# Performance work log

Hardware: AMD Instinct MI355X
Metric: run time of the kernel (lower is better)

## Reference

```python
import jax, jax.numpy as jnp
import numpy as np


def setup_inputs() -> dict:
    key = jax.random.key(0)
    ks = jax.random.split(key, 6)
    B, H, T, Dk, Dv = 64, 16, 4, 128, 256
    q = jax.random.normal(ks[0], (B, H, T, Dk), dtype=jnp.float32)
    k = jax.random.normal(ks[1], (B, H, T, Dk), dtype=jnp.float32)
    v = jax.random.normal(ks[2], (B, H, T, Dv), dtype=jnp.float32)
    g = jax.random.uniform(ks[3], (B, H, T), dtype=jnp.float32)
    beta = jax.random.uniform(ks[4], (B, H, T), dtype=jnp.float32)
    last_recurrent_state = jax.random.normal(ks[5], (B, H, Dk, Dv), dtype=jnp.float32)
    return {"q": q, "k": k, "v": v, "g": g, "beta": beta,
            "last_recurrent_state": last_recurrent_state}


def reference(q, k, v, g, beta, last_recurrent_state):
    # q,k: (B,H,T,Dk)  v: (B,H,T,Dv)  g,beta: (B,H,T)  state: (B,H,Dk,Dv)
    def step(state, xs):
        q_t, k_t, v_t, g_t, beta_t = xs  # (B,H,Dk),(B,H,Dk),(B,H,Dv),(B,H),(B,H)
        state = state * jnp.exp(g_t)[..., None, None]           # decay
        kv_mem = jnp.einsum('bhkv,bhk->bhv', state, k_t)         # readout with key
        delta = (v_t - kv_mem) * beta_t[..., None]               # delta-rule correction
        state = state + k_t[..., None] * delta[..., None, :]     # rank-1 update
        out_t = jnp.einsum('bhkv,bhk->bhv', state, q_t)          # query readout
        return state, out_t

    xs = (jnp.moveaxis(q, 2, 0), jnp.moveaxis(k, 2, 0), jnp.moveaxis(v, 2, 0),
          jnp.moveaxis(g, 2, 0), jnp.moveaxis(beta, 2, 0))
    state, outs = jax.lax.scan(step, last_recurrent_state, xs)
    output = jnp.moveaxis(outs, 0, 2)  # (B,H,T,Dv)
    return jnp.concatenate([output.reshape(-1), state.reshape(-1)], axis=0)
```

## Files before the change

### kernel.cpp

```cpp
#include <hip/hip_runtime.h>

#define BH    1024
#define TT    4
#define DK    128
#define DV    256
#define KSEG  8
#define KLEN  16
#define QV    64


#define PH1(idx, kt)                                   \
    { s4[idx].x *= g_; s4[idx].y *= g_;                \
      s4[idx].z *= g_; s4[idx].w *= g_;                \
      kv.x = fmaf(s4[idx].x, (kt), kv.x);              \
      kv.y = fmaf(s4[idx].y, (kt), kv.y);              \
      kv.z = fmaf(s4[idx].z, (kt), kv.z);              \
      kv.w = fmaf(s4[idx].w, (kt), kv.w); }

#define PH2(idx, kt, qt)                               \
    { s4[idx].x = fmaf((kt), d4.x, s4[idx].x);         \
      s4[idx].y = fmaf((kt), d4.y, s4[idx].y);         \
      s4[idx].z = fmaf((kt), d4.z, s4[idx].z);         \
      s4[idx].w = fmaf((kt), d4.w, s4[idx].w);         \
      o4.x = fmaf(s4[idx].x, (qt), o4.x);              \
      o4.y = fmaf(s4[idx].y, (qt), o4.y);              \
      o4.z = fmaf(s4[idx].z, (qt), o4.z);              \
      o4.w = fmaf(s4[idx].w, (qt), o4.w); }

__global__ __launch_bounds__(128, 4)
void delta_rule_kernel(const float* __restrict__ q,
                       const float* __restrict__ k,
                       const float* __restrict__ v,
                       const float* __restrict__ g,
                       const float* __restrict__ beta,
                       const float* __restrict__ s0,
                       float* __restrict__ out)
{
    const int bx      = blockIdx.x;
    const int bh      = bx >> 2;
    const int quarter = bx & 3;
    const int tid     = threadIdx.x;
    const int kg      = tid & (KSEG - 1);
    const int vg      = tid >> 3;
    const int vcol    = quarter * QV + vg * 4;
    const int kr0     = kg * KLEN;

    const float* __restrict__ sin_p = s0 + (size_t)bh * DK * DV;
    float* __restrict__ out_p  = out + (size_t)bh * TT * DV;
    float* __restrict__ sout_p = out + (size_t)BH * TT * DV + (size_t)bh * DK * DV;

    const float* __restrict__ kbase = k    + (size_t)bh * TT * DK;
    const float* __restrict__ qbase = q    + (size_t)bh * TT * DK;
    const float* __restrict__ vbase = v    + (size_t)bh * TT * DV;
    const float* __restrict__ gbase = g    + (size_t)bh * TT;
    const float* __restrict__ bbase = beta + (size_t)bh * TT;

    float gt[TT], bt[TT];
#pragma unroll
    for (int t = 0; t < TT; ++t) {
        gt[t] = __expf(gbase[t]) ;
        bt[t] = bbase[t];
    }

    float4 s4[KLEN];
#pragma unroll
    for (int kk = 0; kk < KLEN; ++kk)
        s4[kk] = *(const float4*)&sin_p[(size_t)(kr0 + kk) * DV + vcol];

#pragma unroll
    for (int t = 0; t < TT; ++t) {
        float4 kf0 = *(const float4*)&kbase[t * DK + kr0 +  0];
        float4 kf1 = *(const float4*)&kbase[t * DK + kr0 +  4];
        float4 kf2 = *(const float4*)&kbase[t * DK + kr0 +  8];
        float4 kf3 = *(const float4*)&kbase[t * DK + kr0 + 12];
        float4 v4  = *(const float4*)&vbase[t * DV + vcol];

        const float g_ = gt[t];

        float4 kv = make_float4(0.f, 0.f, 0.f, 0.f);
        PH1( 0, kf0.x) PH1( 1, kf0.y) PH1( 2, kf0.z) PH1( 3, kf0.w)
        PH1( 4, kf1.x) PH1( 5, kf1.y) PH1( 6, kf1.z) PH1( 7, kf1.w)
        PH1( 8, kf2.x) PH1( 9, kf2.y) PH1(10, kf2.z) PH1(11, kf2.w)
        PH1(12, kf3.x) PH1(13, kf3.y) PH1(14, kf3.z) PH1(15, kf3.w)

#pragma unroll
        for (int m = 1; m < KSEG; m <<= 1) {
            kv.x += __shfl_xor(kv.x, m);
            kv.y += __shfl_xor(kv.y, m);
            kv.z += __shfl_xor(kv.z, m);
            kv.w += __shfl_xor(kv.w, m);
        }

        float4 d4;
        d4.x = (v4.x - kv.x) * bt[t];
        d4.y = (v4.y - kv.y) * bt[t];
        d4.z = (v4.z - kv.z) * bt[t];
        d4.w = (v4.w - kv.w) * bt[t];

        float4 qf0 = *(const float4*)&qbase[t * DK + kr0 +  0];
        float4 qf1 = *(const float4*)&qbase[t * DK + kr0 +  4];
        float4 qf2 = *(const float4*)&qbase[t * DK + kr0 +  8];
        float4 qf3 = *(const float4*)&qbase[t * DK + kr0 + 12];

        float4 o4 = make_float4(0.f, 0.f, 0.f, 0.f);
        PH2( 0, kf0.x, qf0.x) PH2( 1, kf0.y, qf0.y) PH2( 2, kf0.z, qf0.z) PH2( 3, kf0.w, qf0.w)
        PH2( 4, kf1.x, qf1.x) PH2( 5, kf1.y, qf1.y) PH2( 6, kf1.z, qf1.z) PH2( 7, kf1.w, qf1.w)
        PH2( 8, kf2.x, qf2.x) PH2( 9, kf2.y, qf2.y) PH2(10, kf2.z, qf2.z) PH2(11, kf2.w, qf2.w)
        PH2(12, kf3.x, qf3.x) PH2(13, kf3.y, qf3.y) PH2(14, kf3.z, qf3.z) PH2(15, kf3.w, qf3.w)

#pragma unroll
        for (int m = 1; m < KSEG; m <<= 1) {
            o4.x += __shfl_xor(o4.x, m);
            o4.y += __shfl_xor(o4.y, m);
            o4.z += __shfl_xor(o4.z, m);
            o4.w += __shfl_xor(o4.w, m);
        }
        if (kg == 0)
            *(float4*)&out_p[t * DV + vcol] = o4;
    }

#pragma unroll
    for (int kk = 0; kk < KLEN; ++kk)
        *(float4*)&sout_p[(size_t)(kr0 + kk) * DV + vcol] = s4[kk];
}

extern "C" void kernel_launch(void* const* d_in, const int* in_sizes, int n_in,
                              void* d_out, int out_size, void* d_ws, size_t ws_size,
                              hipStream_t stream) {
    const float* q    = (const float*)d_in[0];
    const float* k    = (const float*)d_in[1];
    const float* v    = (const float*)d_in[2];
    const float* g    = (const float*)d_in[3];
    const float* beta = (const float*)d_in[4];
    const float* s0   = (const float*)d_in[5];
    float* out = (float*)d_out;

    delta_rule_kernel<<<dim3(BH * 4), dim3(128), 0, stream>>>(q, k, v, g, beta, s0, out);
}
```

Measured before the change: 281.8 us.

## Prefetch next-step q/k/v, remap block order, relax launch bounds

Loads the next time step's k, q and v vectors into registers while the current step computes, so global-load latency overlaps the FMA work. Block index mapping changes so consecutive blocks handle different (b,h) pairs for the same quarter instead of four quarters of the same pair. The launch-bounds occupancy hint drops from 4 to 2 blocks to leave room for the extra prefetch registers. These changes trade occupancy and register pressure for latency hiding, and they change L2 locality for the shared k/q reads.

```diff
diff --git a/kernel.cpp b/kernel.cpp
--- a/kernel.cpp
+++ b/kernel.cpp
@@ -27,7 +27,7 @@
       o4.z = fmaf(s4[idx].z, (qt), o4.z);              \
       o4.w = fmaf(s4[idx].w, (qt), o4.w); }
 
-__global__ __launch_bounds__(128, 4)
+__global__ __launch_bounds__(128, 2)
 void delta_rule_kernel(const float* __restrict__ q,
                        const float* __restrict__ k,
                        const float* __restrict__ v,
@@ -37,8 +37,8 @@
                        float* __restrict__ out)
 {
     const int bx      = blockIdx.x;
-    const int bh      = bx >> 2;
-    const int quarter = bx & 3;
+    const int bh      = bx & (BH - 1);
+    const int quarter = bx >> 10;
     const int tid     = threadIdx.x;
     const int kg      = tid & (KSEG - 1);
     const int vg      = tid >> 3;
@@ -49,39 +49,50 @@
     float* __restrict__ out_p  = out + (size_t)bh * TT * DV;
     float* __restrict__ sout_p = out + (size_t)BH * TT * DV + (size_t)bh * DK * DV;
 
-    const float* __restrict__ kbase = k    + (size_t)bh * TT * DK;
-    const float* __restrict__ qbase = q    + (size_t)bh * TT * DK;
-    const float* __restrict__ vbase = v    + (size_t)bh * TT * DV;
+    const float* __restrict__ kbase = k    + (size_t)bh * TT * DK + kr0;
+    const float* __restrict__ qbase = q    + (size_t)bh * TT * DK + kr0;
+    const float* __restrict__ vbase = v    + (size_t)bh * TT * DV + vcol;
     const float* __restrict__ gbase = g    + (size_t)bh * TT;
     const float* __restrict__ bbase = beta + (size_t)bh * TT;
-
-    float gt[TT], bt[TT];
-#pragma unroll
-    for (int t = 0; t < TT; ++t) {
-        gt[t] = __expf(gbase[t]) ;
-        bt[t] = bbase[t];
-    }
 
     float4 s4[KLEN];
 #pragma unroll
     for (int kk = 0; kk < KLEN; ++kk)
         s4[kk] = *(const float4*)&sin_p[(size_t)(kr0 + kk) * DV + vcol];
 
+    float4 kc0 = *(const float4*)&kbase[ 0];
+    float4 kc1 = *(const float4*)&kbase[ 4];
+    float4 kc2 = *(const float4*)&kbase[ 8];
+    float4 kc3 = *(const float4*)&kbase[12];
+    float4 qc0 = *(const float4*)&qbase[ 0];
+    float4 qc1 = *(const float4*)&qbase[ 4];
+    float4 qc2 = *(const float4*)&qbase[ 8];
+    float4 qc3 = *(const float4*)&qbase[12];
+    float4 vc  = *(const float4*)&vbase[0];
+
 #pragma unroll
     for (int t = 0; t < TT; ++t) {
-        float4 kf0 = *(const float4*)&kbase[t * DK + kr0 +  0];
-        float4 kf1 = *(const float4*)&kbase[t * DK + kr0 +  4];
-        float4 kf2 = *(const float4*)&kbase[t * DK + kr0 +  8];
-        float4 kf3 = *(const float4*)&kbase[t * DK + kr0 + 12];
-        float4 v4  = *(const float4*)&vbase[t * DV + vcol];
+        float4 kn0, kn1, kn2, kn3, qn0, qn1, qn2, qn3, vn;
+        if (t < TT - 1) {
+            kn0 = *(const float4*)&kbase[(t + 1) * DK +  0];
+            kn1 = *(const float4*)&kbase[(t + 1) * DK +  4];
+            kn2 = *(const float4*)&kbase[(t + 1) * DK +  8];
+            kn3 = *(const float4*)&kbase[(t + 1) * DK + 12];
+            qn0 = *(const float4*)&qbase[(t + 1) * DK +  0];
+            qn1 = *(const float4*)&qbase[(t + 1) * DK +  4];
+            qn2 = *(const float4*)&qbase[(t + 1) * DK +  8];
+            qn3 = *(const float4*)&qbase[(t + 1) * DK + 12];
+            vn  = *(const float4*)&vbase[(t + 1) * DV];
+        }
 
-        const float g_ = gt[t];
+        const float g_ = __expf(gbase[t]);
+        const float bt = bbase[t];
 
         float4 kv = make_float4(0.f, 0.f, 0.f, 0.f);
-        PH1( 0, kf0.x) PH1( 1, kf0.y) PH1( 2, kf0.z) PH1( 3, kf0.w)
-        PH1( 4, kf1.x) PH1( 5, kf1.y) PH1( 6, kf1.z) PH1( 7, kf1.w)
-        PH1( 8, kf2.x) PH1( 9, kf2.y) PH1(10, kf2.z) PH1(11, kf2.w)
-        PH1(12, kf3.x) PH1(13, kf3.y) PH1(14, kf3.z) PH1(15, kf3.w)
+        PH1( 0, kc0.x) PH1( 1, kc0.y) PH1( 2, kc0.z) PH1( 3, kc0.w)
+        PH1( 4, kc1.x) PH1( 5, kc1.y) PH1( 6, kc1.z) PH1( 7, kc1.w)
+        PH1( 8, kc2.x) PH1( 9, kc2.y) PH1(10, kc2.z) PH1(11, kc2.w)
+        PH1(12, kc3.x) PH1(13, kc3.y) PH1(14, kc3.z) PH1(15, kc3.w)
 
 #pragma unroll
         for (int m = 1; m < KSEG; m <<= 1) {
@@ -92,21 +103,16 @@
         }
 
         float4 d4;
-        d4.x = (v4.x - kv.x) * bt[t];
-        d4.y = (v4.y - kv.y) * bt[t];
-        d4.z = (v4.z - kv.z) * bt[t];
-        d4.w = (v4.w - kv.w) * bt[t];
-
-        float4 qf0 = *(const float4*)&qbase[t * DK + kr0 +  0];
-        float4 qf1 = *(const float4*)&qbase[t * DK + kr0 +  4];
-        float4 qf2 = *(const float4*)&qbase[t * DK + kr0 +  8];
-        float4 qf3 = *(const float4*)&qbase[t * DK + kr0 + 12];
+        d4.x = (vc.x - kv.x) * bt;
+        d4.y = (vc.y - kv.y) * bt;
+        d4.z = (vc.z - kv.z) * bt;
+        d4.w = (vc.w - kv.w) * bt;
 
         float4 o4 = make_float4(0.f, 0.f, 0.f, 0.f);
-        PH2( 0, kf0.x, qf0.x) PH2( 1, kf0.y, qf0.y) PH2( 2, kf0.z, qf0.z) PH2( 3, kf0.w, qf0.w)
-        PH2( 4, kf1.x, qf1.x) PH2( 5, kf1.y, qf1.y) PH2( 6, kf1.z, qf1.z) PH2( 7, kf1.w, qf1.w)
-        PH2( 8, kf2.x, qf2.x) PH2( 9, kf2.y, qf2.y) PH2(10, kf2.z, qf2.z) PH2(11, kf2.w, qf2.w)
-        PH2(12, kf3.x, qf3.x) PH2(13, kf3.y, qf3.y) PH2(14, kf3.z, qf3.z) PH2(15, kf3.w, qf3.w)
+        PH2( 0, kc0.x, qc0.x) PH2( 1, kc0.y, qc0.y) PH2( 2, kc0.z, qc0.z) PH2( 3, kc0.w, qc0.w)
+        PH2( 4, kc1.x, qc1.x) PH2( 5, kc1.y, qc1.y) PH2( 6, kc1.z, qc1.z) PH2( 7, kc1.w, qc1.w)
+        PH2( 8, kc2.x, qc2.x) PH2( 9, kc2.y, qc2.y) PH2(10, kc2.z, qc2.z) PH2(11, kc2.w, qc2.w)
+        PH2(12, kc3.x, qc3.x) PH2(13, kc3.y, qc3.y) PH2(14, kc3.z, qc3.z) PH2(15, kc3.w, qc3.w)
 
 #pragma unroll
         for (int m = 1; m < KSEG; m <<= 1) {
@@ -117,6 +123,12 @@
         }
         if (kg == 0)
             *(float4*)&out_p[t * DV + vcol] = o4;
+
+        if (t < TT - 1) {
+            kc0 = kn0; kc1 = kn1; kc2 = kn2; kc3 = kn3;
+            qc0 = qn0; qc1 = qn1; qc2 = qn2; qc3 = qn3;
+            vc  = vn;
+        }
     }
 
 #pragma unroll
```

New measurement: 270.6 us. 4.0% less time.
